# Optimization experiments

Measured on AMD Instinct MI355X. Metric: run time of the kernel, lower is better.

The kernel has to match this reference:

```python
import jax, jax.numpy as jnp
import numpy as np

B, T, D_IN = 2, 2048, 1024
H, D_HEAD = 16, 64
D_INNER = H * D_HEAD  # 1024
D_OUT = D_HEAD        # out_proj maps d_inner -> d_out


def setup_inputs() -> dict:
    key = jax.random.key(0)
    ks = jax.random.split(key, 6)
    s_in = 1.0 / np.sqrt(D_IN)
    s_inner = 1.0 / np.sqrt(D_INNER)
    return {
        "x": jax.random.normal(ks[0], (B, T, D_IN), dtype=jnp.float32),
        "Wq": jax.random.uniform(ks[1], (D_IN, D_INNER), jnp.float32, -s_in, s_in),
        "Wk": jax.random.uniform(ks[2], (D_IN, D_INNER), jnp.float32, -s_in, s_in),
        "Wv": jax.random.uniform(ks[3], (D_IN, D_INNER), jnp.float32, -s_in, s_in),
        "Wo": jax.random.uniform(ks[4], (D_INNER, D_OUT), jnp.float32, -s_inner, s_inner),
        "bo": jax.random.uniform(ks[5], (D_OUT,), jnp.float32, -s_inner, s_inner),
    }


def reference(x, Wq, Wk, Wv, Wo, bo):
    b, t, _ = x.shape
    # projections -> [b, h, t, d]
    def split_heads(y):
        return y.reshape(b, t, H, D_HEAD).transpose(0, 2, 1, 3)
    q = split_heads(x @ Wq)
    k = split_heads(x @ Wk)
    v = split_heads(x @ Wv)
    scores = jnp.einsum("bhqd,bhkd->bhqk", q, k)
    causal = jnp.triu(jnp.ones((t, t), dtype=bool), k=1)
    scores = jnp.where(causal, -jnp.inf, scores)
    # NOTE: original scales by sqrt(d_out*num_heads), not sqrt(head_dim)
    attn = jax.nn.softmax(scores / np.sqrt(D_INNER), axis=-1)
    y = jnp.einsum("bhqk,bhkd->bhqd", attn, v)
    y = y.transpose(0, 2, 1, 3).reshape(b, t, D_INNER)
    return y @ Wo + bo
```

## Files before the change

kernel.cpp:

```cpp
#include <hip/hip_runtime.h>

typedef __attribute__((ext_vector_type(8))) short short8;
typedef __attribute__((ext_vector_type(4))) float f32x4;
typedef __attribute__((ext_vector_type(8))) unsigned short ushort8v;


__device__ __forceinline__ unsigned short f2bf(float f) {
  union { float f; unsigned int u; } x; x.f = f;
  unsigned int r = x.u + 0x7FFFu + ((x.u >> 16) & 1u);
  return (unsigned short)(r >> 16);
}

__device__ __forceinline__ void gload_lds16(const void* g, void* l) {
  __builtin_amdgcn_global_load_lds(
      (const __attribute__((address_space(1))) void*)g,
      (__attribute__((address_space(3))) void*)l, 16, 0, 0);
}


__global__ __launch_bounds__(256) void prep(
    const float* __restrict__ x,
    const float* __restrict__ Wq, const float* __restrict__ Wk, const float* __restrict__ Wv,
    const float* __restrict__ Wo, const float* __restrict__ bo,
    unsigned short* __restrict__ xb,
    unsigned short* __restrict__ wqt, unsigned short* __restrict__ wkt,
    unsigned short* __restrict__ wvt, unsigned short* __restrict__ wot,
    float* __restrict__ out) {
  __shared__ float tile[32][33];
  int b = blockIdx.x;
  if (b < 4096) {
    int i = (b * 256 + threadIdx.x) * 4;
    float4 f = *(const float4*)(x + i);
    ushort4 o;
    o.x = f2bf(f.x); o.y = f2bf(f.y); o.z = f2bf(f.z); o.w = f2bf(f.w);
    *(ushort4*)(xb + i) = o;
  } else if (b < 7168) {
    int idx = b - 4096;
    int z = idx >> 10, rem = idx & 1023;
    const float* src = (z == 0) ? Wq : (z == 1) ? Wk : Wv;
    unsigned short* dst = (z == 0) ? wqt : (z == 1) ? wkt : wvt;
    int kx = (rem & 31) * 32, ny = (rem >> 5) * 32;
    int tx = threadIdx.x & 31, ty = threadIdx.x >> 5;
    #pragma unroll
    for (int r = 0; r < 32; r += 8)
      tile[ty + r][tx] = src[(size_t)(kx + ty + r) * 1024 + ny + tx];
    __syncthreads();
    #pragma unroll
    for (int r = 0; r < 32; r += 8)
      dst[(size_t)(ny + ty + r) * 1024 + kx + tx] = f2bf(tile[tx][ty + r]);
  } else if (b < 7232) {
    int idx = b - 7168;
    int kx = (idx & 31) * 32, ny = (idx >> 5) * 32;
    int tx = threadIdx.x & 31, ty = threadIdx.x >> 5;
    #pragma unroll
    for (int r = 0; r < 32; r += 8)
      tile[ty + r][tx] = Wo[(size_t)(kx + ty + r) * 64 + ny + tx];
    __syncthreads();
    #pragma unroll
    for (int r = 0; r < 32; r += 8)
      wot[(size_t)(ny + ty + r) * 1024 + kx + tx] = f2bf(tile[tx][ty + r]);
  } else {
    int t = (b - 7232) * 256 + threadIdx.x;
    float4 bi = *(const float4*)(bo + (t & 15) * 4);
    *(float4*)(out + (size_t)t * 4) = bi;
  }
}


__global__ __launch_bounds__(256) void qkv_gemm(
    const unsigned short* __restrict__ Xb,
    const unsigned short* __restrict__ Wqt, const unsigned short* __restrict__ Wkt,
    const unsigned short* __restrict__ Wvt,
    unsigned short* __restrict__ Oq, unsigned short* __restrict__ Ok,
    unsigned short* __restrict__ Ovt) {
  constexpr int Kd = 1024;
  __shared__ __align__(16) unsigned short As[128 * 64];
  __shared__ __align__(16) unsigned short Bs[128 * 64];
  int z = blockIdx.z;
  int m0, n0;
  const unsigned short *Arow, *Brow;
  if (z == 2) {
    m0 = blockIdx.x * 128; n0 = blockIdx.y * 128;
    Arow = Xb; Brow = Wvt;
  } else {
    m0 = blockIdx.y * 128; n0 = blockIdx.x * 128;
    Arow = (z == 0) ? Wqt : Wkt; Brow = Xb;
  }
  int tid = threadIdx.x, lane = tid & 63, wave = tid >> 6;
  int wm = wave >> 1, wn = wave & 1;
  int l15 = lane & 15, quad = lane >> 4;
  int swz = l15 & 7;

  f32x4 acc[4][4] = {};

  for (int k0 = 0; k0 < Kd; k0 += 64) {
    __syncthreads();
    #pragma unroll
    for (int r = 0; r < 4; ++r) {
      int i = tid + 256 * r;
      int row = i >> 3, c8 = i & 7;
      int gc8 = c8 ^ (row & 7);
      gload_lds16(Arow + (size_t)(m0 + row) * Kd + k0 + gc8 * 8, &As[i * 8]);
    }
    #pragma unroll
    for (int r = 0; r < 4; ++r) {
      int i = tid + 256 * r;
      int row = i >> 3, c8 = i & 7;
      int gc8 = c8 ^ (row & 7);
      gload_lds16(Brow + (size_t)(n0 + row) * Kd + k0 + gc8 * 8, &Bs[i * 8]);
    }
    __syncthreads();
    short8 af[4][2], bf[4][2];
    #pragma unroll
    for (int s = 0; s < 2; ++s) {
      #pragma unroll
      for (int i = 0; i < 4; ++i)
        af[i][s] = *(const short8*)&As[(wm * 64 + i * 16 + l15) * 64 + (((s << 2) + quad) ^ swz) * 8];
      #pragma unroll
      for (int j = 0; j < 4; ++j)
        bf[j][s] = *(const short8*)&Bs[(wn * 64 + j * 16 + l15) * 64 + (((s << 2) + quad) ^ swz) * 8];
    }
    #pragma unroll
    for (int s = 0; s < 2; ++s)
      #pragma unroll
      for (int i = 0; i < 4; ++i)
        #pragma unroll
        for (int j = 0; j < 4; ++j)
          acc[i][j] = __builtin_amdgcn_mfma_f32_16x16x32_bf16(af[i][s], bf[j][s], acc[i][j], 0, 0, 0);
  }

  if (z == 2) {
    #pragma unroll
    for (int i = 0; i < 4; ++i) {
      int tbase = m0 + wm * 64 + i * 16 + quad * 4;
      int b = tbase >> 11, tt = tbase & 2047;
      #pragma unroll
      for (int j = 0; j < 4; ++j) {
        int dm = n0 + wn * 64 + j * 16 + l15;
        int h = dm >> 6, d = dm & 63;
        unsigned int u0 = f2bf(acc[i][j][0]), u1 = f2bf(acc[i][j][1]);
        unsigned int u2 = f2bf(acc[i][j][2]), u3 = f2bf(acc[i][j][3]);
        uint2 pk; pk.x = u0 | (u1 << 16); pk.y = u2 | (u3 << 16);
        *(uint2*)(Ovt + (((size_t)(b * 16 + h) * 64 + d) << 11) + tt) = pk;
      }
    }
  } else {
    unsigned short* O = (z == 0) ? Oq : Ok;
    float scale = (z == 0) ? 0.03125f : 1.0f;
    #pragma unroll
    for (int i = 0; i < 4; ++i) {
      int dmbase = m0 + wm * 64 + i * 16 + quad * 4;
      int h = dmbase >> 6, d0 = dmbase & 63;
      #pragma unroll
      for (int j = 0; j < 4; ++j) {
        int t = n0 + wn * 64 + j * 16 + l15;
        int b = t >> 11, tt = t & 2047;
        unsigned int u0 = f2bf(acc[i][j][0] * scale), u1 = f2bf(acc[i][j][1] * scale);
        unsigned int u2 = f2bf(acc[i][j][2] * scale), u3 = f2bf(acc[i][j][3] * scale);
        uint2 pk; pk.x = u0 | (u1 << 16); pk.y = u2 | (u3 << 16);
        *(uint2*)(O + (((size_t)(b * 16 + h) * 2048 + tt) << 6) + d0) = pk;
      }
    }
  }
}


__global__ __launch_bounds__(256, 2) void attn9(
    const unsigned short* __restrict__ Qg, const unsigned short* __restrict__ Kg,
    const unsigned short* __restrict__ Vtg, unsigned short* __restrict__ Yg) {
  constexpr int T = 2048;
  __shared__ __align__(16) unsigned short Ks[64 * 72];
  __shared__ __align__(16) unsigned short Vs[64 * 72];
  __shared__ __align__(16) unsigned short Ps[4][32 * 72];
  int bh = blockIdx.x;
  int by = blockIdx.y;
  int pp = (by < 8) ? by : 23 - by;
  int qtA = pp, qtB = 31 - pp;
  int tid = threadIdx.x, lane = tid & 63, wave = tid >> 6;
  int l15 = lane & 15, quad = lane >> 4;
  const unsigned short* Qb = Qg + (size_t)bh * T * 64;
  const unsigned short* Kb = Kg + (size_t)bh * T * 64;
  const unsigned short* Vb = Vtg + (size_t)bh * 64 * T;
  int h = bh & 15, b = bh >> 4;
  int qw[2] = {qtA * 64 + wave * 16, qtB * 64 + wave * 16};

  short8 qf[2][2];
  #pragma unroll
  for (int jq = 0; jq < 2; ++jq)
    #pragma unroll
    for (int s = 0; s < 2; ++s)
      qf[jq][s] = *(const short8*)(Qb + (size_t)(qw[jq] + l15) * 64 + quad * 8 + 32 * s);

  f32x4 Oacc[2][4] = {};
  float m_run[2] = {-__builtin_inff(), -__builtin_inff()};
  float l_run[2] = {0.f, 0.f};

  ushort8v kpre[2], vpre[2];
  #pragma unroll
  for (int r = 0; r < 2; ++r) {
    int i = tid + 256 * r;
    kpre[r] = *(const ushort8v*)(Kb + (size_t)(i >> 3) * 64 + (i & 7) * 8);
    vpre[r] = *(const ushort8v*)(Vb + (size_t)(i >> 3) * T + (i & 7) * 8);
  }

  for (int kt = 0; kt <= qtA; ++kt) {
    __syncthreads();
    #pragma unroll
    for (int r = 0; r < 2; ++r) {
      int i = tid + 256 * r;
      *(ushort8v*)&Ks[(i >> 3) * 72 + (i & 7) * 8] = kpre[r];
      *(ushort8v*)&Vs[(i >> 3) * 72 + (i & 7) * 8] = vpre[r];
    }
    __syncthreads();
    {
      #pragma unroll
      for (int r = 0; r < 2; ++r) {
        int i = tid + 256 * r;
        kpre[r] = *(const ushort8v*)(Kb + (size_t)((kt + 1) * 64 + (i >> 3)) * 64 + (i & 7) * 8);
        vpre[r] = *(const ushort8v*)(Vb + (size_t)(i >> 3) * T + (kt + 1) * 64 + (i & 7) * 8);
      }
    }

    f32x4 S[4][2] = {};
    #pragma unroll
    for (int s = 0; s < 2; ++s)
      #pragma unroll
      for (int mi = 0; mi < 4; ++mi) {
        short8 kf = *(const short8*)&Ks[(mi * 16 + l15) * 72 + quad * 8 + 32 * s];
        #pragma unroll
        for (int jq = 0; jq < 2; ++jq)
          S[mi][jq] = __builtin_amdgcn_mfma_f32_16x16x32_bf16(kf, qf[jq][s], S[mi][jq], 0, 0, 0);
      }

    if (kt == qtA) {
      int ql = wave * 16 + l15;
      #pragma unroll
      for (int mi = 0; mi < 4; ++mi) {
        int tokl = mi * 16 + quad * 4;
        #pragma unroll
        for (int r = 0; r < 4; ++r)
          if (tokl + r > ql) S[mi][0][r] = -__builtin_inff();
      }
    }

    float alpha[2];
    #pragma unroll
    for (int jq = 0; jq < 2; ++jq) {
      float vmax = -__builtin_inff();
      #pragma unroll
      for (int mi = 0; mi < 4; ++mi)
        #pragma unroll
        for (int r = 0; r < 4; ++r)
          vmax = fmaxf(vmax, S[mi][jq][r]);
      vmax = fmaxf(vmax, __shfl_xor(vmax, 16));
      vmax = fmaxf(vmax, __shfl_xor(vmax, 32));
      float mnew = fmaxf(m_run[jq], vmax);
      alpha[jq] = __expf(m_run[jq] - mnew);
      m_run[jq] = mnew;
      float rs = 0.f;
      #pragma unroll
      for (int mi = 0; mi < 4; ++mi) {
        float p0 = __expf(S[mi][jq][0] - mnew);
        float p1 = __expf(S[mi][jq][1] - mnew);
        float p2 = __expf(S[mi][jq][2] - mnew);
        float p3 = __expf(S[mi][jq][3] - mnew);
        rs += (p0 + p1) + (p2 + p3);
        union { float f; unsigned int u; } a0{p0}, a1{p1}, a2{p2}, a3{p3};
        uint2 pk;
        pk.x = ((a0.u + 0x8000u) >> 16) | ((a1.u + 0x8000u) & 0xFFFF0000u);
        pk.y = ((a2.u + 0x8000u) >> 16) | ((a3.u + 0x8000u) & 0xFFFF0000u);
        *(uint2*)&Ps[wave][(jq * 16 + l15) * 72 + mi * 16 + quad * 4] = pk;
      }
      rs += __shfl_xor(rs, 16);
      rs += __shfl_xor(rs, 32);
      l_run[jq] = l_run[jq] * alpha[jq] + rs;
    }

    #pragma unroll
    for (int jq = 0; jq < 2; ++jq)
      #pragma unroll
      for (int jd = 0; jd < 4; ++jd)
        #pragma unroll
        for (int r = 0; r < 4; ++r)
          Oacc[jq][jd][r] *= alpha[jq];

    #pragma unroll
    for (int s = 0; s < 2; ++s) {
      short8 vfr[4];
      #pragma unroll
      for (int jd = 0; jd < 4; ++jd)
        vfr[jd] = *(const short8*)&Vs[(jd * 16 + l15) * 72 + s * 32 + quad * 8];
      #pragma unroll
      for (int jq = 0; jq < 2; ++jq) {
        short8 pf = *(const short8*)&Ps[wave][(jq * 16 + l15) * 72 + s * 32 + quad * 8];
        #pragma unroll
        for (int jd = 0; jd < 4; ++jd)
          Oacc[jq][jd] = __builtin_amdgcn_mfma_f32_16x16x32_bf16(vfr[jd], pf, Oacc[jq][jd], 0, 0, 0);
      }
    }
  }

  for (int kt = qtA + 1; kt <= qtB; ++kt) {
    __syncthreads();
    #pragma unroll
    for (int r = 0; r < 2; ++r) {
      int i = tid + 256 * r;
      *(ushort8v*)&Ks[(i >> 3) * 72 + (i & 7) * 8] = kpre[r];
      *(ushort8v*)&Vs[(i >> 3) * 72 + (i & 7) * 8] = vpre[r];
    }
    __syncthreads();
    if (kt < qtB) {
      #pragma unroll
      for (int r = 0; r < 2; ++r) {
        int i = tid + 256 * r;
        kpre[r] = *(const ushort8v*)(Kb + (size_t)((kt + 1) * 64 + (i >> 3)) * 64 + (i & 7) * 8);
        vpre[r] = *(const ushort8v*)(Vb + (size_t)(i >> 3) * T + (kt + 1) * 64 + (i & 7) * 8);
      }
    }

    f32x4 S[4] = {};
    #pragma unroll
    for (int s = 0; s < 2; ++s)
      #pragma unroll
      for (int mi = 0; mi < 4; ++mi) {
        short8 kf = *(const short8*)&Ks[(mi * 16 + l15) * 72 + quad * 8 + 32 * s];
        S[mi] = __builtin_amdgcn_mfma_f32_16x16x32_bf16(kf, qf[1][s], S[mi], 0, 0, 0);
      }

    if (kt == qtB) {
      int ql = wave * 16 + l15;
      #pragma unroll
      for (int mi = 0; mi < 4; ++mi) {
        int tokl = mi * 16 + quad * 4;
        #pragma unroll
        for (int r = 0; r < 4; ++r)
          if (tokl + r > ql) S[mi][r] = -__builtin_inff();
      }
    }

    float vmax = -__builtin_inff();
    #pragma unroll
    for (int mi = 0; mi < 4; ++mi)
      #pragma unroll
      for (int r = 0; r < 4; ++r)
        vmax = fmaxf(vmax, S[mi][r]);
    vmax = fmaxf(vmax, __shfl_xor(vmax, 16));
    vmax = fmaxf(vmax, __shfl_xor(vmax, 32));
    float mnew = fmaxf(m_run[1], vmax);
    float alpha = __expf(m_run[1] - mnew);
    m_run[1] = mnew;
    float rs = 0.f;
    #pragma unroll
    for (int mi = 0; mi < 4; ++mi) {
      float p0 = __expf(S[mi][0] - mnew);
      float p1 = __expf(S[mi][1] - mnew);
      float p2 = __expf(S[mi][2] - mnew);
      float p3 = __expf(S[mi][3] - mnew);
      rs += (p0 + p1) + (p2 + p3);
      union { float f; unsigned int u; } a0{p0}, a1{p1}, a2{p2}, a3{p3};
      uint2 pk;
      pk.x = ((a0.u + 0x8000u) >> 16) | ((a1.u + 0x8000u) & 0xFFFF0000u);
      pk.y = ((a2.u + 0x8000u) >> 16) | ((a3.u + 0x8000u) & 0xFFFF0000u);
      *(uint2*)&Ps[wave][(16 + l15) * 72 + mi * 16 + quad * 4] = pk;
    }
    rs += __shfl_xor(rs, 16);
    rs += __shfl_xor(rs, 32);
    l_run[1] = l_run[1] * alpha + rs;

    #pragma unroll
    for (int jd = 0; jd < 4; ++jd)
      #pragma unroll
      for (int r = 0; r < 4; ++r)
        Oacc[1][jd][r] *= alpha;

    #pragma unroll
    for (int s = 0; s < 2; ++s) {
      short8 pf = *(const short8*)&Ps[wave][(16 + l15) * 72 + s * 32 + quad * 8];
      #pragma unroll
      for (int jd = 0; jd < 4; ++jd) {
        short8 vfr = *(const short8*)&Vs[(jd * 16 + l15) * 72 + s * 32 + quad * 8];
        Oacc[1][jd] = __builtin_amdgcn_mfma_f32_16x16x32_bf16(vfr, pf, Oacc[1][jd], 0, 0, 0);
      }
    }
  }

  #pragma unroll
  for (int jq = 0; jq < 2; ++jq) {
    float linv = 1.f / l_run[jq];
    int q = qw[jq] + l15;
    size_t row = (size_t)(b * 2048 + q) * 1024 + h * 64 + quad * 4;
    #pragma unroll
    for (int jd = 0; jd < 4; ++jd) {
      unsigned int u0 = f2bf(Oacc[jq][jd][0] * linv), u1 = f2bf(Oacc[jq][jd][1] * linv);
      unsigned int u2 = f2bf(Oacc[jq][jd][2] * linv), u3 = f2bf(Oacc[jq][jd][3] * linv);
      uint2 pk; pk.x = u0 | (u1 << 16); pk.y = u2 | (u3 << 16);
      *(uint2*)(Yg + row + jd * 16) = pk;
    }
  }
}


__global__ __launch_bounds__(256) void oproj(
    const unsigned short* __restrict__ Y, const unsigned short* __restrict__ Wot,
    float* __restrict__ out) {
  __shared__ __align__(16) unsigned short As[64 * 32];
  __shared__ __align__(16) unsigned short Bs[64 * 32];
  int m0 = blockIdx.x * 64;
  int kbase = blockIdx.y * 256;
  int tid = threadIdx.x, lane = tid & 63, wave = tid >> 6;
  int l15 = lane & 15, quad = lane >> 4;
  f32x4 acc[4] = {};
  for (int k0 = kbase; k0 < kbase + 256; k0 += 32) {
    __syncthreads();
    {
      int row = tid >> 2, c8 = (tid & 3) * 8;
      gload_lds16(Y + (size_t)(m0 + row) * 1024 + k0 + c8, &As[tid * 8]);
      gload_lds16(Wot + (size_t)row * 1024 + k0 + c8, &Bs[tid * 8]);
    }
    __syncthreads();
    short8 af = *(const short8*)&As[(wave * 16 + l15) * 32 + quad * 8];
    #pragma unroll
    for (int j = 0; j < 4; ++j) {
      short8 bf = *(const short8*)&Bs[(j * 16 + l15) * 32 + quad * 8];
      acc[j] = __builtin_amdgcn_mfma_f32_16x16x32_bf16(af, bf, acc[j], 0, 0, 0);
    }
  }
  #pragma unroll
  for (int j = 0; j < 4; ++j) {
    int n = j * 16 + l15;
    #pragma unroll
    for (int r = 0; r < 4; ++r) {
      int m = m0 + wave * 16 + quad * 4 + r;
      atomicAdd(&out[(size_t)m * 64 + n], acc[j][r]);
    }
  }
}


extern "C" void kernel_launch(void* const* d_in, const int* in_sizes, int n_in,
                              void* d_out, int out_size, void* d_ws, size_t ws_size,
                              hipStream_t stream) {
  const float* x  = (const float*)d_in[0];
  const float* Wq = (const float*)d_in[1];
  const float* Wk = (const float*)d_in[2];
  const float* Wv = (const float*)d_in[3];
  const float* Wo = (const float*)d_in[4];
  const float* bo = (const float*)d_in[5];
  float* out = (float*)d_out;
  char* ws = (char*)d_ws;

  unsigned short* xb  = (unsigned short*)(ws);
  unsigned short* wqt = (unsigned short*)(ws + (8ull << 20));
  unsigned short* wkt = (unsigned short*)(ws + (10ull << 20));
  unsigned short* wvt = (unsigned short*)(ws + (12ull << 20));
  unsigned short* wot = (unsigned short*)(ws + (14ull << 20));
  unsigned short* q   = (unsigned short*)(ws + (15ull << 20));
  unsigned short* k   = (unsigned short*)(ws + (23ull << 20));
  unsigned short* vt  = (unsigned short*)(ws + (31ull << 20));
  unsigned short* y   = (unsigned short*)(ws + (39ull << 20));

  prep<<<7488, 256, 0, stream>>>(x, Wq, Wk, Wv, Wo, bo, xb, wqt, wkt, wvt, wot, out);
  qkv_gemm<<<dim3(32, 8, 3), 256, 0, stream>>>(xb, wqt, wkt, wvt, q, k, vt);
  attn9<<<dim3(32, 16), 256, 0, stream>>>(q, k, vt, y);
  oproj<<<dim3(64, 4), 256, 0, stream>>>(y, wot, out);
}
```

Baseline: 165.8 us.

## Double-buffer K/V in LDS with XOR swizzle, exp2 softmax and lazy rescaling

Result: no change. 163.0 us (-1.7%).

```diff
diff --git a/kernel.cpp b/kernel.cpp
--- a/kernel.cpp
+++ b/kernel.cpp
@@ -146,7 +146,7 @@
     }
   } else {
     unsigned short* O = (z == 0) ? Oq : Ok;
-    float scale = (z == 0) ? 0.03125f : 1.0f;
+    float scale = (z == 0) ? 0.0450842200f : 1.0f;
     #pragma unroll
     for (int i = 0; i < 4; ++i) {
       int dmbase = m0 + wm * 64 + i * 16 + quad * 4;
@@ -165,19 +165,20 @@
 }
 
 
-__global__ __launch_bounds__(256, 2) void attn9(
+__global__ __launch_bounds__(256, 2) void attn10(
     const unsigned short* __restrict__ Qg, const unsigned short* __restrict__ Kg,
     const unsigned short* __restrict__ Vtg, unsigned short* __restrict__ Yg) {
   constexpr int T = 2048;
-  __shared__ __align__(16) unsigned short Ks[64 * 72];
-  __shared__ __align__(16) unsigned short Vs[64 * 72];
-  __shared__ __align__(16) unsigned short Ps[4][32 * 72];
+  __shared__ __align__(16) unsigned short Ks[2][64 * 64];
+  __shared__ __align__(16) unsigned short Vs[2][64 * 64];
+  __shared__ __align__(16) unsigned short Ps[4][32 * 64];
   int bh = blockIdx.x;
   int by = blockIdx.y;
   int pp = (by < 8) ? by : 23 - by;
   int qtA = pp, qtB = 31 - pp;
   int tid = threadIdx.x, lane = tid & 63, wave = tid >> 6;
   int l15 = lane & 15, quad = lane >> 4;
+  int swz = l15 & 7;
   const unsigned short* Qb = Qg + (size_t)bh * T * 64;
   const unsigned short* Kb = Kg + (size_t)bh * T * 64;
   const unsigned short* Vb = Vtg + (size_t)bh * 64 * T;
@@ -195,42 +196,45 @@
   float m_run[2] = {-__builtin_inff(), -__builtin_inff()};
   float l_run[2] = {0.f, 0.f};
 
+  int srow = tid >> 3, sc8 = tid & 7;
+  int sdst = srow * 64 + ((sc8 ^ (srow & 7)) * 8);
+
   ushort8v kpre[2], vpre[2];
   #pragma unroll
   for (int r = 0; r < 2; ++r) {
-    int i = tid + 256 * r;
-    kpre[r] = *(const ushort8v*)(Kb + (size_t)(i >> 3) * 64 + (i & 7) * 8);
-    vpre[r] = *(const ushort8v*)(Vb + (size_t)(i >> 3) * T + (i & 7) * 8);
-  }
+    kpre[r] = *(const ushort8v*)(Kb + (size_t)(srow + 32 * r) * 64 + sc8 * 8);
+    vpre[r] = *(const ushort8v*)(Vb + (size_t)(srow + 32 * r) * T + sc8 * 8);
+  }
+  *(ushort8v*)&Ks[0][sdst] = kpre[0];
+  *(ushort8v*)&Ks[0][sdst + 2048] = kpre[1];
+  *(ushort8v*)&Vs[0][sdst] = vpre[0];
+  *(ushort8v*)&Vs[0][sdst + 2048] = vpre[1];
+  __syncthreads();
 
   for (int kt = 0; kt <= qtA; ++kt) {
-    __syncthreads();
+    const unsigned short* Kl = Ks[kt & 1];
+    const unsigned short* Vl = Vs[kt & 1];
+    unsigned short* Kn = Ks[(kt & 1) ^ 1];
+    unsigned short* Vn = Vs[(kt & 1) ^ 1];
+
     #pragma unroll
     for (int r = 0; r < 2; ++r) {
-      int i = tid + 256 * r;
-      *(ushort8v*)&Ks[(i >> 3) * 72 + (i & 7) * 8] = kpre[r];
-      *(ushort8v*)&Vs[(i >> 3) * 72 + (i & 7) * 8] = vpre[r];
-    }
-    __syncthreads();
-    {
-      #pragma unroll
-      for (int r = 0; r < 2; ++r) {
-        int i = tid + 256 * r;
-        kpre[r] = *(const ushort8v*)(Kb + (size_t)((kt + 1) * 64 + (i >> 3)) * 64 + (i & 7) * 8);
-        vpre[r] = *(const ushort8v*)(Vb + (size_t)(i >> 3) * T + (kt + 1) * 64 + (i & 7) * 8);
-      }
+      kpre[r] = *(const ushort8v*)(Kb + (size_t)((kt + 1) * 64 + srow + 32 * r) * 64 + sc8 * 8);
+      vpre[r] = *(const ushort8v*)(Vb + (size_t)(srow + 32 * r) * T + (kt + 1) * 64 + sc8 * 8);
     }
 
     f32x4 S[4][2] = {};
+    __builtin_amdgcn_s_setprio(1);
     #pragma unroll
     for (int s = 0; s < 2; ++s)
       #pragma unroll
       for (int mi = 0; mi < 4; ++mi) {
-        short8 kf = *(const short8*)&Ks[(mi * 16 + l15) * 72 + quad * 8 + 32 * s];
+        short8 kf = *(const short8*)&Kl[(mi * 16 + l15) * 64 + ((quad + 4 * s) ^ swz) * 8];
         #pragma unroll
         for (int jq = 0; jq < 2; ++jq)
           S[mi][jq] = __builtin_amdgcn_mfma_f32_16x16x32_bf16(kf, qf[jq][s], S[mi][jq], 0, 0, 0);
       }
+    __builtin_amdgcn_s_setprio(0);
 
     if (kt == qtA) {
       int ql = wave * 16 + l15;
@@ -243,33 +247,36 @@
       }
     }
 
-    float alpha[2];
+    float alpha[2]; bool norescale[2];
     #pragma unroll
     for (int jq = 0; jq < 2; ++jq) {
-      float vmax = -__builtin_inff();
-      #pragma unroll
-      for (int mi = 0; mi < 4; ++mi)
-        #pragma unroll
-        for (int r = 0; r < 4; ++r)
-          vmax = fmaxf(vmax, S[mi][jq][r]);
+      float t0 = fmaxf(fmaxf(S[0][jq][0], S[0][jq][1]), fmaxf(S[0][jq][2], S[0][jq][3]));
+      float t1 = fmaxf(fmaxf(S[1][jq][0], S[1][jq][1]), fmaxf(S[1][jq][2], S[1][jq][3]));
+      float t2 = fmaxf(fmaxf(S[2][jq][0], S[2][jq][1]), fmaxf(S[2][jq][2], S[2][jq][3]));
+      float t3 = fmaxf(fmaxf(S[3][jq][0], S[3][jq][1]), fmaxf(S[3][jq][2], S[3][jq][3]));
+      float vmax = fmaxf(fmaxf(t0, t1), fmaxf(t2, t3));
       vmax = fmaxf(vmax, __shfl_xor(vmax, 16));
       vmax = fmaxf(vmax, __shfl_xor(vmax, 32));
-      float mnew = fmaxf(m_run[jq], vmax);
-      alpha[jq] = __expf(m_run[jq] - mnew);
+      float mold = m_run[jq];
+      bool defer = __all(vmax - mold <= 8.f) != 0;
+      float mnew = defer ? mold : fmaxf(mold, vmax);
+      alpha[jq] = defer ? 1.f : __builtin_amdgcn_exp2f(mold - mnew);
+      norescale[jq] = defer;
       m_run[jq] = mnew;
       float rs = 0.f;
       #pragma unroll
       for (int mi = 0; mi < 4; ++mi) {
-        float p0 = __expf(S[mi][jq][0] - mnew);
-        float p1 = __expf(S[mi][jq][1] - mnew);
-        float p2 = __expf(S[mi][jq][2] - mnew);
-        float p3 = __expf(S[mi][jq][3] - mnew);
+        float p0 = __builtin_amdgcn_exp2f(S[mi][jq][0] - mnew);
+        float p1 = __builtin_amdgcn_exp2f(S[mi][jq][1] - mnew);
+        float p2 = __builtin_amdgcn_exp2f(S[mi][jq][2] - mnew);
+        float p3 = __builtin_amdgcn_exp2f(S[mi][jq][3] - mnew);
         rs += (p0 + p1) + (p2 + p3);
         union { float f; unsigned int u; } a0{p0}, a1{p1}, a2{p2}, a3{p3};
         uint2 pk;
         pk.x = ((a0.u + 0x8000u) >> 16) | ((a1.u + 0x8000u) & 0xFFFF0000u);
         pk.y = ((a2.u + 0x8000u) >> 16) | ((a3.u + 0x8000u) & 0xFFFF0000u);
-        *(uint2*)&Ps[wave][(jq * 16 + l15) * 72 + mi * 16 + quad * 4] = pk;
+        int g = (2 * mi + (quad >> 1)) ^ swz;
+        *(uint2*)&Ps[wave][(jq * 16 + l15) * 64 + g * 8 + (quad & 1) * 4] = pk;
       }
       rs += __shfl_xor(rs, 16);
       rs += __shfl_xor(rs, 32);
@@ -278,54 +285,61 @@
 
     #pragma unroll
     for (int jq = 0; jq < 2; ++jq)
-      #pragma unroll
-      for (int jd = 0; jd < 4; ++jd)
-        #pragma unroll
-        for (int r = 0; r < 4; ++r)
-          Oacc[jq][jd][r] *= alpha[jq];
-
+      if (!norescale[jq])
+        #pragma unroll
+        for (int jd = 0; jd < 4; ++jd)
+          #pragma unroll
+          for (int r = 0; r < 4; ++r)
+            Oacc[jq][jd][r] *= alpha[jq];
+
+    *(ushort8v*)&Kn[sdst] = kpre[0];
+    *(ushort8v*)&Kn[sdst + 2048] = kpre[1];
+    *(ushort8v*)&Vn[sdst] = vpre[0];
+    *(ushort8v*)&Vn[sdst + 2048] = vpre[1];
+
+    __builtin_amdgcn_s_setprio(1);
     #pragma unroll
     for (int s = 0; s < 2; ++s) {
       short8 vfr[4];
       #pragma unroll
       for (int jd = 0; jd < 4; ++jd)
-        vfr[jd] = *(const short8*)&Vs[(jd * 16 + l15) * 72 + s * 32 + quad * 8];
+        vfr[jd] = *(const short8*)&Vl[(jd * 16 + l15) * 64 + ((quad + 4 * s) ^ swz) * 8];
       #pragma unroll
       for (int jq = 0; jq < 2; ++jq) {
-        short8 pf = *(const short8*)&Ps[wave][(jq * 16 + l15) * 72 + s * 32 + quad * 8];
+        short8 pf = *(const short8*)&Ps[wave][(jq * 16 + l15) * 64 + ((quad + 4 * s) ^ swz) * 8];
         #pragma unroll
         for (int jd = 0; jd < 4; ++jd)
           Oacc[jq][jd] = __builtin_amdgcn_mfma_f32_16x16x32_bf16(vfr[jd], pf, Oacc[jq][jd], 0, 0, 0);
       }
     }
+    __builtin_amdgcn_s_setprio(0);
+    __syncthreads();
   }
 
   for (int kt = qtA + 1; kt <= qtB; ++kt) {
-    __syncthreads();
-    #pragma unroll
-    for (int r = 0; r < 2; ++r) {
-      int i = tid + 256 * r;
-      *(ushort8v*)&Ks[(i >> 3) * 72 + (i & 7) * 8] = kpre[r];
-      *(ushort8v*)&Vs[(i >> 3) * 72 + (i & 7) * 8] = vpre[r];
-    }
-    __syncthreads();
+    const unsigned short* Kl = Ks[kt & 1];
+    const unsigned short* Vl = Vs[kt & 1];
+    unsigned short* Kn = Ks[(kt & 1) ^ 1];
+    unsigned short* Vn = Vs[(kt & 1) ^ 1];
+
     if (kt < qtB) {
       #pragma unroll
       for (int r = 0; r < 2; ++r) {
-        int i = tid + 256 * r;
-        kpre[r] = *(const ushort8v*)(Kb + (size_t)((kt + 1) * 64 + (i >> 3)) * 64 + (i & 7) * 8);
-        vpre[r] = *(const ushort8v*)(Vb + (size_t)(i >> 3) * T + (kt + 1) * 64 + (i & 7) * 8);
+        kpre[r] = *(const ushort8v*)(Kb + (size_t)((kt + 1) * 64 + srow + 32 * r) * 64 + sc8 * 8);
+        vpre[r] = *(const ushort8v*)(Vb + (size_t)(srow + 32 * r) * T + (kt + 1) * 64 + sc8 * 8);
       }
     }
 
     f32x4 S[4] = {};
+    __builtin_amdgcn_s_setprio(1);
     #pragma unroll
     for (int s = 0; s < 2; ++s)
       #pragma unroll
       for (int mi = 0; mi < 4; ++mi) {
-        short8 kf = *(const short8*)&Ks[(mi * 16 + l15) * 72 + quad * 8 + 32 * s];
+        short8 kf = *(const short8*)&Kl[(mi * 16 + l15) * 64 + ((quad + 4 * s) ^ swz) * 8];
         S[mi] = __builtin_amdgcn_mfma_f32_16x16x32_bf16(kf, qf[1][s], S[mi], 0, 0, 0);
       }
+    __builtin_amdgcn_s_setprio(0);
 
     if (kt == qtB) {
       int ql = wave * 16 + l15;
@@ -338,50 +352,63 @@
       }
     }
 
-    float vmax = -__builtin_inff();
-    #pragma unroll
-    for (int mi = 0; mi < 4; ++mi)
-      #pragma unroll
-      for (int r = 0; r < 4; ++r)
-        vmax = fmaxf(vmax, S[mi][r]);
+    float t0 = fmaxf(fmaxf(S[0][0], S[0][1]), fmaxf(S[0][2], S[0][3]));
+    float t1 = fmaxf(fmaxf(S[1][0], S[1][1]), fmaxf(S[1][2], S[1][3]));
+    float t2 = fmaxf(fmaxf(S[2][0], S[2][1]), fmaxf(S[2][2], S[2][3]));
+    float t3 = fmaxf(fmaxf(S[3][0], S[3][1]), fmaxf(S[3][2], S[3][3]));
+    float vmax = fmaxf(fmaxf(t0, t1), fmaxf(t2, t3));
     vmax = fmaxf(vmax, __shfl_xor(vmax, 16));
     vmax = fmaxf(vmax, __shfl_xor(vmax, 32));
-    float mnew = fmaxf(m_run[1], vmax);
-    float alpha = __expf(m_run[1] - mnew);
+    float mold = m_run[1];
+    bool defer = __all(vmax - mold <= 8.f) != 0;
+    float mnew = defer ? mold : fmaxf(mold, vmax);
+    float alpha = defer ? 1.f : __builtin_amdgcn_exp2f(mold - mnew);
     m_run[1] = mnew;
     float rs = 0.f;
     #pragma unroll
     for (int mi = 0; mi < 4; ++mi) {
-      float p0 = __expf(S[mi][0] - mnew);
-      float p1 = __expf(S[mi][1] - mnew);
-      float p2 = __expf(S[mi][2] - mnew);
-      float p3 = __expf(S[mi][3] - mnew);
+      float p0 = __builtin_amdgcn_exp2f(S[mi][0] - mnew);
+      float p1 = __builtin_amdgcn_exp2f(S[mi][1] - mnew);
+      float p2 = __builtin_amdgcn_exp2f(S[mi][2] - mnew);
+      float p3 = __builtin_amdgcn_exp2f(S[mi][3] - mnew);
       rs += (p0 + p1) + (p2 + p3);
       union { float f; unsigned int u; } a0{p0}, a1{p1}, a2{p2}, a3{p3};
       uint2 pk;
       pk.x = ((a0.u + 0x8000u) >> 16) | ((a1.u + 0x8000u) & 0xFFFF0000u);
       pk.y = ((a2.u + 0x8000u) >> 16) | ((a3.u + 0x8000u) & 0xFFFF0000u);
-      *(uint2*)&Ps[wave][(16 + l15) * 72 + mi * 16 + quad * 4] = pk;
+      int g = (2 * mi + (quad >> 1)) ^ swz;
+      *(uint2*)&Ps[wave][(16 + l15) * 64 + g * 8 + (quad & 1) * 4] = pk;
     }
     rs += __shfl_xor(rs, 16);
     rs += __shfl_xor(rs, 32);
     l_run[1] = l_run[1] * alpha + rs;
 
-    #pragma unroll
-    for (int jd = 0; jd < 4; ++jd)
-      #pragma unroll
-      for (int r = 0; r < 4; ++r)
-        Oacc[1][jd][r] *= alpha;
-
+    if (!defer)
+      #pragma unroll
+      for (int jd = 0; jd < 4; ++jd)
+        #pragma unroll
+        for (int r = 0; r < 4; ++r)
+          Oacc[1][jd][r] *= alpha;
+
+    if (kt < qtB) {
+      *(ushort8v*)&Kn[sdst] = kpre[0];
+      *(ushort8v*)&Kn[sdst + 2048] = kpre[1];
+      *(ushort8v*)&Vn[sdst] = vpre[0];
+      *(ushort8v*)&Vn[sdst + 2048] = vpre[1];
+    }
+
+    __builtin_amdgcn_s_setprio(1);
     #pragma unroll
     for (int s = 0; s < 2; ++s) {
-      short8 pf = *(const short8*)&Ps[wave][(16 + l15) * 72 + s * 32 + quad * 8];
+      short8 pf = *(const short8*)&Ps[wave][(16 + l15) * 64 + ((quad + 4 * s) ^ swz) * 8];
       #pragma unroll
       for (int jd = 0; jd < 4; ++jd) {
-        short8 vfr = *(const short8*)&Vs[(jd * 16 + l15) * 72 + s * 32 + quad * 8];
+        short8 vfr = *(const short8*)&Vl[(jd * 16 + l15) * 64 + ((quad + 4 * s) ^ swz) * 8];
         Oacc[1][jd] = __builtin_amdgcn_mfma_f32_16x16x32_bf16(vfr, pf, Oacc[1][jd], 0, 0, 0);
       }
     }
+    __builtin_amdgcn_s_setprio(0);
+    __syncthreads();
   }
 
   #pragma unroll
@@ -461,6 +488,6 @@
 
   prep<<<7488, 256, 0, stream>>>(x, Wq, Wk, Wv, Wo, bo, xb, wqt, wkt, wvt, wot, out);
   qkv_gemm<<<dim3(32, 8, 3), 256, 0, stream>>>(xb, wqt, wkt, wvt, q, k, vt);
-  attn9<<<dim3(32, 16), 256, 0, stream>>>(q, k, vt, y);
+  attn10<<<dim3(32, 16), 256, 0, stream>>>(q, k, vt, y);
   oproj<<<dim3(64, 4), 256, 0, stream>>>(y, wot, out);
 }
```
